# Kernel optimization log

Hardware: AMD Instinct MI355X
Metric: run time of the kernel (lower is better)

Reference implementation:

```python
import jax, jax.numpy as jnp
import numpy as np

MARGIN = 1.0
B, D, NUM_CLASSES = 8192, 128, 10


def setup_inputs() -> dict:
    key = jax.random.key(0)
    k1, k2 = jax.random.split(key)
    embeddings = jax.random.normal(k1, (B, D), dtype=jnp.float32)
    labels = jax.random.randint(k2, (B,), 0, NUM_CLASSES, dtype=jnp.int64)
    return {"embeddings": embeddings, "labels": labels}


def reference(embeddings, labels):
    # pairwise Euclidean distances d[i, j] = sqrt(sum((e_i - e_j)^2))
    sq = jnp.sum(embeddings * embeddings, axis=-1)               # [B]
    d2 = sq[:, None] + sq[None, :] - 2.0 * (embeddings @ embeddings.T)
    dist = jnp.sqrt(jnp.maximum(d2, 0.0))                        # [B, B]

    same = labels[:, None] == labels[None, :]                    # [B, B] bool
    neg_inf = jnp.float32(-jnp.inf)
    pos_inf = jnp.float32(jnp.inf)

    # hardest positive: max distance among same-class (includes self, dist 0, harmless)
    hardest_pos = jnp.max(jnp.where(same, dist, neg_inf), axis=1)   # [B]
    # hardest negative: min distance among different-class
    hardest_neg = jnp.min(jnp.where(same, pos_inf, dist), axis=1)   # [B]

    per_anchor = jax.nn.relu(hardest_pos - hardest_neg + MARGIN)    # [B]
    # use_gt_than_zero_mean=False -> divide by batch size
    return jnp.sum(per_anchor) / per_anchor.shape[0]
```

## Files before the change

kernel.cpp:

```cpp
#include <hip/hip_runtime.h>
#include <hip/hip_bf16.h>
#include <cstdint>

#define BATCH 8192
#define DIM   128
#define KAUG  160
#define MARGIN 1.0f
#define SEP    8192.0f

typedef __attribute__((ext_vector_type(8))) short short8;
typedef __attribute__((ext_vector_type(4))) float f32x4;

__device__ __forceinline__ void async_copy16(const void* g, void* lds) {
    __builtin_amdgcn_global_load_lds(
        (const __attribute__((address_space(1))) unsigned int*)g,
        (__attribute__((address_space(3))) unsigned int*)lds, 16, 0, 0);
}

__global__ __launch_bounds__(256) void bhtl_prep(
    const float* __restrict__ emb,
    const int* __restrict__ labels,
    __hip_bfloat16* __restrict__ EbfA,
    __hip_bfloat16* __restrict__ EbfB,
    float* __restrict__ sq,
    unsigned* __restrict__ hp2,
    unsigned* __restrict__ hn2)
{
    const int w   = threadIdx.x >> 6;
    const int l   = threadIdx.x & 63;
    const int row = blockIdx.x * 4 + w;
    const float2 e = ((const float2*)(emb + row * DIM))[l];
    __hip_bfloat162 h2;
    h2.x = __float2bfloat16(e.x);
    h2.y = __float2bfloat16(e.y);
    ((__hip_bfloat162*)(EbfA + (size_t)row * KAUG))[l] = h2;
    ((__hip_bfloat162*)(EbfB + (size_t)row * KAUG))[l] = h2;
    if (l < 16) {
        const int lab = labels[row];
        const float a0 = (2 * l     == lab) ? 64.f : 0.f;
        const float a1 = (2 * l + 1 == lab) ? 64.f : 0.f;
        __hip_bfloat162 hA, hB;
        hA.x = __float2bfloat16(a0);  hA.y = __float2bfloat16(a1);
        hB.x = __float2bfloat16(-a0); hB.y = __float2bfloat16(-a1);
        ((__hip_bfloat162*)(EbfA + (size_t)row * KAUG + DIM))[l] = hA;
        ((__hip_bfloat162*)(EbfB + (size_t)row * KAUG + DIM))[l] = hB;
    }
    float s = e.x * e.x + e.y * e.y;
    #pragma unroll
    for (int d = 1; d < 64; d <<= 1) s += __shfl_xor(s, d, 64);
    if (l == 0) {
        sq[row]  = s;
        hp2[row] = 0u;
        hn2[row] = 0x7F800000u;
    }
}

__global__ __launch_bounds__(128) void bhtl_main(
    const __hip_bfloat16* __restrict__ EbfA,
    const __hip_bfloat16* __restrict__ EbfB,
    const float* __restrict__ sq,
    unsigned* __restrict__ hp2,
    unsigned* __restrict__ hn2)
{
    __shared__ __align__(16) unsigned short B_s[5][2560];
    __shared__ __align__(16) float sqm[512];

    const int tid  = threadIdx.x;
    const int w    = tid >> 6;
    const int lane = tid & 63;
    const int q    = lane >> 4;
    const int ln   = lane & 15;
    const int rt   = blockIdx.x >> 4;
    const int js   = blockIdx.x & 15;
    const int rowbase = rt * 128 + w * 64;
    const int jbase   = js * 512;

    auto stageB = [&](int buf, int ch) {
        const int jb = jbase + ch * 16;
        #pragma unroll
        for (int c = 0; c < 5; ++c) {
            int U   = c * 64 + lane;
            int col = U / 20;
            int u   = U - col * 20;
            int g   = (u < 16) ? (u ^ (col & 7)) : u;
            async_copy16(EbfB + (size_t)(jb + col) * KAUG + g * 8,
                         &B_s[buf][c * 512]);
        }
    };

    short8 af[4][5];
    float  sqi[4];
    #pragma unroll
    for (int m = 0; m < 4; ++m) {
        const int row = rowbase + m * 16 + ln;
        #pragma unroll
        for (int kc = 0; kc < 5; ++kc) {
            af[m][kc] = *(const short8*)(EbfA + (size_t)row * KAUG + kc * 32 + q * 8);
            asm("" : "+v"(af[m][kc]));
        }
        sqi[m] = sq[row];
    }

    if (w == 0) {
        async_copy16(sq + jbase +       lane * 4, &sqm[0]);
        async_copy16(sq + jbase + 256 + lane * 4, &sqm[256]);
    }
    stageB(w,     w);
    stageB(w + 2, w + 2);
    asm volatile("s_waitcnt vmcnt(0)" ::: "memory");
    asm volatile("s_barrier" ::: "memory");

    float mp[4] = {-INFINITY, -INFINITY, -INFINITY, -INFINITY};
    float mn[4] = { INFINITY,  INFINITY,  INFINITY,  INFINITY};

    auto doIter = [&](int i, int buf, int par, bool doStage, int stageBuf,
                      bool finalWait) {
        if (par == w) {
            if (finalWait) asm volatile("s_waitcnt vmcnt(0)" ::: "memory");
            else           asm volatile("s_waitcnt vmcnt(5)" ::: "memory");
        }
        asm volatile("s_barrier" ::: "memory");

        short8 bfr[5];
        #pragma unroll
        for (int kc = 0; kc < 5; ++kc) {
            const int t    = kc * 4 + q;
            const int unit = (kc < 4) ? (t ^ (ln & 7)) : t;
            bfr[kc] = *(const short8*)(&B_s[buf][(ln * 20 + unit) * 8]);
        }
        f32x4 sqj = *(const f32x4*)(&sqm[i * 16 + q * 4]);

        if (doStage && par == w) stageB(stageBuf, i + 4);

        f32x4 acc[4];
        const f32x4 zero = {0.f, 0.f, 0.f, 0.f};
        #pragma unroll
        for (int m = 0; m < 4; ++m) acc[m] = zero;
        #pragma unroll
        for (int kc = 0; kc < 5; ++kc)
            #pragma unroll
            for (int m = 0; m < 4; ++m)
                acc[m] = __builtin_amdgcn_mfma_f32_16x16x32_bf16(
                    bfr[kc], af[m][kc], acc[m], 0, 0, 0);

        #pragma unroll
        for (int m = 0; m < 4; ++m)
            #pragma unroll
            for (int r = 0; r < 4; ++r) {
                float val = fmaf(-2.0f, acc[m][r], sqj[r]);
                mp[m] = fmaxf(mp[m], val);
                mn[m] = fminf(mn[m], val);
            }
    };

    #pragma unroll 1
    for (int base = 0; base < 30; base += 10) {
        #pragma unroll
        for (int k = 0; k < 10; ++k) {
            const int i = base + k;
            doIter(i, k % 5, k & 1, i <= 27, (k + 4) % 5, false);
        }
    }
    doIter(30, 0, 0, false, 0, true);
    doIter(31, 1, 1, false, 0, true);

    #pragma unroll
    for (int m = 0; m < 4; ++m) {
        float a = mp[m], b = mn[m];
        a = fmaxf(a, __shfl_xor(a, 16, 64));
        a = fmaxf(a, __shfl_xor(a, 32, 64));
        b = fminf(b, __shfl_xor(b, 16, 64));
        b = fminf(b, __shfl_xor(b, 32, 64));
        if (q == 0) {
            const int row = rowbase + m * 16 + ln;
            atomicMax(&hp2[row], __float_as_uint(fmaxf(sqi[m] + a - SEP, 0.0f)));
            atomicMin(&hn2[row], __float_as_uint(fmaxf(sqi[m] + b, 0.0f)));
        }
    }
}

__global__ __launch_bounds__(1024) void bhtl_final(
    const unsigned* __restrict__ hp2,
    const unsigned* __restrict__ hn2,
    float* __restrict__ out)
{
    __shared__ float red[16];
    float sum = 0.f;
    for (int i = threadIdx.x; i < BATCH; i += 1024) {
        float hp = sqrtf(__uint_as_float(hp2[i]));
        float hn = sqrtf(__uint_as_float(hn2[i]));
        sum += fmaxf(hp - hn + MARGIN, 0.f);
    }
    #pragma unroll
    for (int d = 1; d < 64; d <<= 1) sum += __shfl_xor(sum, d, 64);
    int wv = threadIdx.x >> 6;
    if ((threadIdx.x & 63) == 0) red[wv] = sum;
    __syncthreads();
    if (threadIdx.x < 64) {
        float v = (threadIdx.x < 16) ? red[threadIdx.x] : 0.f;
        #pragma unroll
        for (int d = 1; d < 16; d <<= 1) v += __shfl_xor(v, d, 64);
        if (threadIdx.x == 0) out[0] = v / (float)BATCH;
    }
}

extern "C" void kernel_launch(void* const* d_in, const int* in_sizes, int n_in,
                              void* d_out, int out_size, void* d_ws, size_t ws_size,
                              hipStream_t stream)
{
    const float* emb    = (const float*)d_in[0];
    const int*   labels = (const int*)d_in[1];
    float*       out    = (float*)d_out;

    char* ws = (char*)d_ws;
    __hip_bfloat16* EbfA = (__hip_bfloat16*)ws;
    __hip_bfloat16* EbfB = (__hip_bfloat16*)(ws + 3  * 1024 * 1024);
    float*    sq   = (float*)   (ws + 6 * 1024 * 1024);
    unsigned* hp2  = (unsigned*)(ws + 6 * 1024 * 1024 + 32 * 1024);
    unsigned* hn2  = (unsigned*)(ws + 6 * 1024 * 1024 + 64 * 1024);

    bhtl_prep<<<BATCH / 4, 256, 0, stream>>>(emb, labels, EbfA, EbfB, sq, hp2, hn2);
    bhtl_main<<<1024, 128, 0, stream>>>(EbfA, EbfB, sq, hp2, hn2);
    bhtl_final<<<1, 1024, 0, stream>>>(hp2, hn2, out);
}
```

Baseline: 95.92 us.

## Exploit distance-matrix symmetry with upper-triangular 128x128 tiles and column reductions

The main kernel now launches 2080 blocks, each owning one 128x128 tile of the upper triangle of the pairwise matrix, instead of 1024 blocks that each cover 128 rows by 512 columns. Each off-diagonal tile also reduces per-column max/min through shared memory and updates the column anchors with atomics, which roughly halves the MFMA work. The whole B tile is loaded once up front, replacing the multi-buffered async pipeline. The cost is extra cross-lane shuffles, twice as many atomics, and a triangular index computation using sqrt, and loads no longer overlap with compute.

Measured after the change: 104.4 us. +8.8%, slower.

```diff
diff --git a/kernel.cpp b/kernel.cpp
--- a/kernel.cpp
+++ b/kernel.cpp
@@ -62,31 +62,42 @@
     unsigned* __restrict__ hp2,
     unsigned* __restrict__ hn2)
 {
-    __shared__ __align__(16) unsigned short B_s[5][2560];
-    __shared__ __align__(16) float sqm[512];
+    __shared__ __align__(16) unsigned short B_s[20480];
+    __shared__ __align__(16) float sqm[256];
+    __shared__ float cmaxS[2][128];
+    __shared__ float cminS[2][128];
 
     const int tid  = threadIdx.x;
     const int w    = tid >> 6;
     const int lane = tid & 63;
     const int q    = lane >> 4;
     const int ln   = lane & 15;
-    const int rt   = blockIdx.x >> 4;
-    const int js   = blockIdx.x & 15;
+
+    const int bid = blockIdx.x;
+    int rt = (int)floorf((129.0f - sqrtf(16641.0f - 8.0f * (float)bid)) * 0.5f);
+    {
+        int Tr = (rt * (129 - rt)) >> 1;
+        int Tn = ((rt + 1) * (128 - rt)) >> 1;
+        if (bid < Tr)      rt -= 1;
+        else if (bid >= Tn) rt += 1;
+    }
+    const int Trt = (rt * (129 - rt)) >> 1;
+    const int ct  = rt + (bid - Trt);
+    const bool offd = (rt != ct);
     const int rowbase = rt * 128 + w * 64;
-    const int jbase   = js * 512;
-
-    auto stageB = [&](int buf, int ch) {
-        const int jb = jbase + ch * 16;
-        #pragma unroll
-        for (int c = 0; c < 5; ++c) {
-            int U   = c * 64 + lane;
-            int col = U / 20;
-            int u   = U - col * 20;
-            int g   = (u < 16) ? (u ^ (col & 7)) : u;
-            async_copy16(EbfB + (size_t)(jb + col) * KAUG + g * 8,
-                         &B_s[buf][c * 512]);
-        }
-    };
+    const int colbase = ct * 128;
+
+    #pragma unroll
+    for (int c = 0; c < 20; ++c) {
+        int U   = w * 1280 + c * 64 + lane;
+        int col = U / 20;
+        int u   = U - col * 20;
+        int g   = (u < 16) ? (u ^ (col & 7)) : u;
+        async_copy16(EbfB + (size_t)(colbase + col) * KAUG + g * 8,
+                     &B_s[(w * 1280 + c * 64) * 8]);
+    }
+    if (w == 0)
+        async_copy16(sq + colbase + (lane & 31) * 4, &sqm[0]);
 
     short8 af[4][5];
     float  sqi[4];
@@ -101,36 +112,21 @@
         sqi[m] = sq[row];
     }
 
-    if (w == 0) {
-        async_copy16(sq + jbase +       lane * 4, &sqm[0]);
-        async_copy16(sq + jbase + 256 + lane * 4, &sqm[256]);
-    }
-    stageB(w,     w);
-    stageB(w + 2, w + 2);
-    asm volatile("s_waitcnt vmcnt(0)" ::: "memory");
-    asm volatile("s_barrier" ::: "memory");
+    __syncthreads();
 
     float mp[4] = {-INFINITY, -INFINITY, -INFINITY, -INFINITY};
     float mn[4] = { INFINITY,  INFINITY,  INFINITY,  INFINITY};
 
-    auto doIter = [&](int i, int buf, int par, bool doStage, int stageBuf,
-                      bool finalWait) {
-        if (par == w) {
-            if (finalWait) asm volatile("s_waitcnt vmcnt(0)" ::: "memory");
-            else           asm volatile("s_waitcnt vmcnt(5)" ::: "memory");
-        }
-        asm volatile("s_barrier" ::: "memory");
-
+    #pragma unroll 2
+    for (int ch = 0; ch < 8; ++ch) {
         short8 bfr[5];
         #pragma unroll
         for (int kc = 0; kc < 5; ++kc) {
             const int t    = kc * 4 + q;
-            const int unit = (kc < 4) ? (t ^ (ln & 7)) : t;
-            bfr[kc] = *(const short8*)(&B_s[buf][(ln * 20 + unit) * 8]);
-        }
-        f32x4 sqj = *(const f32x4*)(&sqm[i * 16 + q * 4]);
-
-        if (doStage && par == w) stageB(stageBuf, i + 4);
+            const int unit = (t < 16) ? (t ^ (ln & 7)) : t;
+            bfr[kc] = *(const short8*)(&B_s[((ch * 16 + ln) * 20 + unit) * 8]);
+        }
+        f32x4 sqj = *(const f32x4*)(&sqm[ch * 16 + q * 4]);
 
         f32x4 acc[4];
         const f32x4 zero = {0.f, 0.f, 0.f, 0.f};
@@ -151,19 +147,36 @@
                 mp[m] = fmaxf(mp[m], val);
                 mn[m] = fminf(mn[m], val);
             }
-    };
-
-    #pragma unroll 1
-    for (int base = 0; base < 30; base += 10) {
-        #pragma unroll
-        for (int k = 0; k < 10; ++k) {
-            const int i = base + k;
-            doIter(i, k % 5, k & 1, i <= 27, (k + 4) % 5, false);
-        }
-    }
-    doIter(30, 0, 0, false, 0, true);
-    doIter(31, 1, 1, false, 0, true);
-
+
+        if (offd) {
+            float cmx[4], cmn[4];
+            #pragma unroll
+            for (int r = 0; r < 4; ++r) {
+                float v0 = fmaf(-2.0f, acc[0][r], sqi[0]);
+                float v1 = fmaf(-2.0f, acc[1][r], sqi[1]);
+                float v2 = fmaf(-2.0f, acc[2][r], sqi[2]);
+                float v3 = fmaf(-2.0f, acc[3][r], sqi[3]);
+                cmx[r] = fmaxf(fmaxf(v0, v1), fmaxf(v2, v3));
+                cmn[r] = fminf(fminf(v0, v1), fminf(v2, v3));
+            }
+            #pragma unroll
+            for (int r = 0; r < 4; ++r)
+                #pragma unroll
+                for (int d = 1; d < 16; d <<= 1) {
+                    cmx[r] = fmaxf(cmx[r], __shfl_xor(cmx[r], d, 64));
+                    cmn[r] = fminf(cmn[r], __shfl_xor(cmn[r], d, 64));
+                }
+            if (ln == 0) {
+                #pragma unroll
+                for (int r = 0; r < 4; ++r) {
+                    cmaxS[w][ch * 16 + q * 4 + r] = cmx[r];
+                    cminS[w][ch * 16 + q * 4 + r] = cmn[r];
+                }
+            }
+        }
+    }
+
+    float rhp[4], rhn[4];
     #pragma unroll
     for (int m = 0; m < 4; ++m) {
         float a = mp[m], b = mn[m];
@@ -171,12 +184,28 @@
         a = fmaxf(a, __shfl_xor(a, 32, 64));
         b = fminf(b, __shfl_xor(b, 16, 64));
         b = fminf(b, __shfl_xor(b, 32, 64));
+        rhp[m] = fmaxf(sqi[m] + a - SEP, 0.0f);
+        rhn[m] = fmaxf(sqi[m] + b, 0.0f);
+    }
+
+    __syncthreads();
+
+    if (offd) {
+        const int ccol = tid;
+        float a  = fmaxf(cmaxS[0][ccol], cmaxS[1][ccol]);
+        float b  = fminf(cminS[0][ccol], cminS[1][ccol]);
+        float sj = sqm[ccol];
+        atomicMax(&hp2[colbase + ccol], __float_as_uint(fmaxf(sj + a - SEP, 0.0f)));
+        atomicMin(&hn2[colbase + ccol], __float_as_uint(fmaxf(sj + b, 0.0f)));
+    }
+
+    #pragma unroll
+    for (int m = 0; m < 4; ++m)
         if (q == 0) {
             const int row = rowbase + m * 16 + ln;
-            atomicMax(&hp2[row], __float_as_uint(fmaxf(sqi[m] + a - SEP, 0.0f)));
-            atomicMin(&hn2[row], __float_as_uint(fmaxf(sqi[m] + b, 0.0f)));
-        }
-    }
+            atomicMax(&hp2[row], __float_as_uint(rhp[m]));
+            atomicMin(&hn2[row], __float_as_uint(rhn[m]));
+        }
 }
 
 __global__ __launch_bounds__(1024) void bhtl_final(
@@ -220,6 +249,6 @@
     unsigned* hn2  = (unsigned*)(ws + 6 * 1024 * 1024 + 64 * 1024);
 
     bhtl_prep<<<BATCH / 4, 256, 0, stream>>>(emb, labels, EbfA, EbfB, sq, hp2, hn2);
-    bhtl_main<<<1024, 128, 0, stream>>>(EbfA, EbfB, sq, hp2, hn2);
+    bhtl_main<<<2080, 128, 0, stream>>>(EbfA, EbfB, sq, hp2, hn2);
     bhtl_final<<<1, 1024, 0, stream>>>(hp2, hn2, out);
 }
```

## Replace LDS-staged B tiles with direct global register loads in smaller blocks

Applied to the files above, without the earlier changes.

Drops the shared-memory staging of B columns via async global-to-LDS copies and barriers. Each single-wave block now loads B fragments and squared norms straight from global memory into registers, double-buffering them in registers. The tile shrinks from 128 to 32 rows per block, so the grid grows fourfold. This removes barrier and LDS traffic but gives up reuse of B across waves, increasing global/L2 read traffic and per-wave MFMA work per load.

After: 110.4 us. 15.0% more time.

```diff
diff --git a/kernel.cpp b/kernel.cpp
--- a/kernel.cpp
+++ b/kernel.cpp
@@ -10,12 +10,6 @@
 
 typedef __attribute__((ext_vector_type(8))) short short8;
 typedef __attribute__((ext_vector_type(4))) float f32x4;
-
-__device__ __forceinline__ void async_copy16(const void* g, void* lds) {
-    __builtin_amdgcn_global_load_lds(
-        (const __attribute__((address_space(1))) unsigned int*)g,
-        (__attribute__((address_space(3))) unsigned int*)lds, 16, 0, 0);
-}
 
 __global__ __launch_bounds__(256) void bhtl_prep(
     const float* __restrict__ emb,
@@ -55,43 +49,26 @@
     }
 }
 
-__global__ __launch_bounds__(128) void bhtl_main(
+__global__ __launch_bounds__(64, 4) void bhtl_main(
     const __hip_bfloat16* __restrict__ EbfA,
     const __hip_bfloat16* __restrict__ EbfB,
     const float* __restrict__ sq,
     unsigned* __restrict__ hp2,
     unsigned* __restrict__ hn2)
 {
-    __shared__ __align__(16) unsigned short B_s[5][2560];
-    __shared__ __align__(16) float sqm[512];
-
-    const int tid  = threadIdx.x;
-    const int w    = tid >> 6;
-    const int lane = tid & 63;
+    const int lane = threadIdx.x;
     const int q    = lane >> 4;
     const int ln   = lane & 15;
-    const int rt   = blockIdx.x >> 4;
-    const int js   = blockIdx.x & 15;
-    const int rowbase = rt * 128 + w * 64;
+    const int bid  = blockIdx.x;
+    const int js   = bid & 15;
+    const int rb   = bid >> 4;
+    const int rowbase = rb * 32;
     const int jbase   = js * 512;
 
-    auto stageB = [&](int buf, int ch) {
-        const int jb = jbase + ch * 16;
-        #pragma unroll
-        for (int c = 0; c < 5; ++c) {
-            int U   = c * 64 + lane;
-            int col = U / 20;
-            int u   = U - col * 20;
-            int g   = (u < 16) ? (u ^ (col & 7)) : u;
-            async_copy16(EbfB + (size_t)(jb + col) * KAUG + g * 8,
-                         &B_s[buf][c * 512]);
-        }
-    };
-
-    short8 af[4][5];
-    float  sqi[4];
+    short8 af[2][5];
+    float  sqi[2];
     #pragma unroll
-    for (int m = 0; m < 4; ++m) {
+    for (int m = 0; m < 2; ++m) {
         const int row = rowbase + m * 16 + ln;
         #pragma unroll
         for (int kc = 0; kc < 5; ++kc) {
@@ -101,71 +78,50 @@
         sqi[m] = sq[row];
     }
 
-    if (w == 0) {
-        async_copy16(sq + jbase +       lane * 4, &sqm[0]);
-        async_copy16(sq + jbase + 256 + lane * 4, &sqm[256]);
-    }
-    stageB(w,     w);
-    stageB(w + 2, w + 2);
-    asm volatile("s_waitcnt vmcnt(0)" ::: "memory");
-    asm volatile("s_barrier" ::: "memory");
+    float mp[2] = {-INFINITY, -INFINITY};
+    float mn[2] = { INFINITY,  INFINITY};
 
-    float mp[4] = {-INFINITY, -INFINITY, -INFINITY, -INFINITY};
-    float mn[4] = { INFINITY,  INFINITY,  INFINITY,  INFINITY};
+    auto loadB = [&](short8 (&bf)[5], f32x4& sj, int ch) {
+        const int jb = jbase + ch * 16;
+        #pragma unroll
+        for (int kc = 0; kc < 5; ++kc)
+            bf[kc] = *(const short8*)(EbfB + (size_t)(jb + ln) * KAUG + kc * 32 + q * 8);
+        sj = *(const f32x4*)(sq + jb + q * 4);
+    };
 
-    auto doIter = [&](int i, int buf, int par, bool doStage, int stageBuf,
-                      bool finalWait) {
-        if (par == w) {
-            if (finalWait) asm volatile("s_waitcnt vmcnt(0)" ::: "memory");
-            else           asm volatile("s_waitcnt vmcnt(5)" ::: "memory");
-        }
-        asm volatile("s_barrier" ::: "memory");
-
-        short8 bfr[5];
-        #pragma unroll
-        for (int kc = 0; kc < 5; ++kc) {
-            const int t    = kc * 4 + q;
-            const int unit = (kc < 4) ? (t ^ (ln & 7)) : t;
-            bfr[kc] = *(const short8*)(&B_s[buf][(ln * 20 + unit) * 8]);
-        }
-        f32x4 sqj = *(const f32x4*)(&sqm[i * 16 + q * 4]);
-
-        if (doStage && par == w) stageB(stageBuf, i + 4);
-
-        f32x4 acc[4];
+    auto compute = [&](const short8 (&bf)[5], const f32x4& sj) {
+        f32x4 acc[2];
         const f32x4 zero = {0.f, 0.f, 0.f, 0.f};
-        #pragma unroll
-        for (int m = 0; m < 4; ++m) acc[m] = zero;
+        acc[0] = zero; acc[1] = zero;
         #pragma unroll
         for (int kc = 0; kc < 5; ++kc)
             #pragma unroll
-            for (int m = 0; m < 4; ++m)
+            for (int m = 0; m < 2; ++m)
                 acc[m] = __builtin_amdgcn_mfma_f32_16x16x32_bf16(
-                    bfr[kc], af[m][kc], acc[m], 0, 0, 0);
-
+                    bf[kc], af[m][kc], acc[m], 0, 0, 0);
         #pragma unroll
-        for (int m = 0; m < 4; ++m)
+        for (int m = 0; m < 2; ++m)
             #pragma unroll
             for (int r = 0; r < 4; ++r) {
-                float val = fmaf(-2.0f, acc[m][r], sqj[r]);
+                float val = fmaf(-2.0f, acc[m][r], sj[r]);
                 mp[m] = fmaxf(mp[m], val);
                 mn[m] = fminf(mn[m], val);
             }
     };
 
+    short8 b0[5], b1[5];
+    f32x4  s0, s1;
+    loadB(b0, s0, 0);
     #pragma unroll 1
-    for (int base = 0; base < 30; base += 10) {
-        #pragma unroll
-        for (int k = 0; k < 10; ++k) {
-            const int i = base + k;
-            doIter(i, k % 5, k & 1, i <= 27, (k + 4) % 5, false);
-        }
+    for (int ch = 0; ch < 32; ch += 2) {
+        loadB(b1, s1, ch + 1);
+        compute(b0, s0);
+        if (ch + 2 < 32) loadB(b0, s0, ch + 2);
+        compute(b1, s1);
     }
-    doIter(30, 0, 0, false, 0, true);
-    doIter(31, 1, 1, false, 0, true);
 
     #pragma unroll
-    for (int m = 0; m < 4; ++m) {
+    for (int m = 0; m < 2; ++m) {
         float a = mp[m], b = mn[m];
         a = fmaxf(a, __shfl_xor(a, 16, 64));
         a = fmaxf(a, __shfl_xor(a, 32, 64));
@@ -220,6 +176,6 @@
     unsigned* hn2  = (unsigned*)(ws + 6 * 1024 * 1024 + 64 * 1024);
 
     bhtl_prep<<<BATCH / 4, 256, 0, stream>>>(emb, labels, EbfA, EbfB, sq, hp2, hn2);
-    bhtl_main<<<1024, 128, 0, stream>>>(EbfA, EbfB, sq, hp2, hn2);
+    bhtl_main<<<4096, 64, 0, stream>>>(EbfA, EbfB, sq, hp2, hn2);
     bhtl_final<<<1, 1024, 0, stream>>>(hp2, hn2, out);
 }
```
